# Kernel optimization log

Hardware: AMD Instinct MI355X
Metric: run time of the kernel (lower is better)

The kernel has to match this reference:

```python
import jax, jax.numpy as jnp
import numpy as np

B, G, C, H = 32, 512, 384, 768
TAU = 0.1
ITERS = 10


def _xavier(key, shape):
    fan_in, fan_out = shape
    lim = (6.0 / (fan_in + fan_out)) ** 0.5
    return jax.random.uniform(key, shape, minval=-lim, maxval=lim, dtype=jnp.float32)


def setup_inputs() -> dict:
    key = jax.random.key(0)
    ks = jax.random.split(key, 4)
    return {
        "center_coords": jax.random.normal(ks[0], (B, G, 3), dtype=jnp.float32),
        "group_features": jax.random.normal(ks[1], (B, G, C), dtype=jnp.float32),
        "W1": _xavier(ks[2], (C, H)),
        "b1": jnp.zeros((H,), jnp.float32),
        "W2": _xavier(ks[3], (H, G)),
        "b2": jnp.zeros((G,), jnp.float32),
    }


def _sinkhorn(scores):
    # scores: (B, G, G); log-space Sinkhorn row/col normalization
    log_alpha = scores / TAU
    for _ in range(ITERS):
        log_alpha = log_alpha - jax.nn.logsumexp(log_alpha, axis=-1, keepdims=True)
        log_alpha = log_alpha - jax.nn.logsumexp(log_alpha, axis=-2, keepdims=True)
    return jnp.exp(log_alpha)


def _greedy_assign(P):
    # Equivalent to torch loop: process entries in descending value order,
    # assign (row, col) if both free == repeatedly take global argmax over
    # entries with free row and free col. P: (G, G) -> perm: (G,) int32.
    g = P.shape[-1]
    flat = P.reshape(-1)

    def step(_, carry):
        row_free, col_free, assign = carry
        mask = (row_free[:, None] & col_free[None, :]).reshape(-1)
        idx = jnp.argmax(jnp.where(mask, flat, -jnp.inf))
        r = idx // g
        c = idx % g
        return (row_free.at[r].set(False), col_free.at[c].set(False), assign.at[r].set(c.astype(jnp.int32)))

    init = (jnp.ones((g,), bool), jnp.ones((g,), bool), jnp.full((g,), -1, jnp.int32))
    _, _, assign = jax.lax.fori_loop(0, g, step, init)
    return assign


def _apply_perm(data, perm):
    # reordered[new_pos] = data[orig_pos]; perm[orig_pos] = new_pos
    return jnp.zeros_like(data).at[perm].set(data)


def reference(center_coords, group_features, W1, b1, W2, b2):
    h = jax.nn.relu(jnp.einsum('bgc,ch->bgh', group_features, W1) + b1)
    scores = jnp.einsum('bgh,hk->bgk', h, W2) + b2  # (B, G, G)
    P = _sinkhorn(scores)
    perm_indices = jax.vmap(_greedy_assign)(P)  # (B, G)
    reordered_coords = jax.vmap(_apply_perm)(center_coords, perm_indices)
    reordered_feats = jax.vmap(_apply_perm)(group_features, perm_indices)
    return reordered_coords, reordered_feats, perm_indices
```

## Files before the change

### kernel.cpp

```cpp
#include <hip/hip_runtime.h>
#include <math.h>

#define NB 32
#define NG 512
#define NC 384
#define NH 768

typedef float f32x4v __attribute__((ext_vector_type(4)));
typedef __bf16 bf16_t;
typedef bf16_t bf16x8 __attribute__((ext_vector_type(8)));
typedef bf16_t bf16x4 __attribute__((ext_vector_type(4)));

__device__ __forceinline__ void split3(float x, bf16_t& h, bf16_t& m, bf16_t& lo)
{
    h = (bf16_t)x;
    float r1 = x - (float)h;
    m = (bf16_t)r1;
    float r2 = r1 - (float)m;
    lo = (bf16_t)r2;
}

__global__ __launch_bounds__(256) void presplit_W(
    const float* __restrict__ W, bf16_t* __restrict__ planeB, int K, int N)
{
    int tid = blockIdx.x * 256 + threadIdx.x;
    int nkc = K >> 5;
    if (tid >= nkc * N) return;
    int kc = tid / N;
    int col = tid - kc * N;
    bf16x8 rh[4], rm[4], rl[4];
#pragma unroll
    for (int k = 0; k < 32; k++) {
        float x = W[(size_t)(kc * 32 + k) * N + col];
        bf16_t h, m, lo;
        split3(x, h, m, lo);
        const int s = (k >> 2) & 3;
        const int sub = ((k >> 4) << 2) + (k & 3);
        rh[s][sub] = h; rm[s][sub] = m; rl[s][sub] = lo;
    }
    int swz = (col >> 1) & 3;
    size_t b0 = ((size_t)(kc * 3 + 0) * N + col) * 32;
    size_t b1 = ((size_t)(kc * 3 + 1) * N + col) * 32;
    size_t b2 = ((size_t)(kc * 3 + 2) * N + col) * 32;
#pragma unroll
    for (int s = 0; s < 4; s++) {
        int d = (s ^ swz) << 3;
        *(bf16x8*)&planeB[b0 + d] = rh[s];
        *(bf16x8*)&planeB[b1 + d] = rm[s];
        *(bf16x8*)&planeB[b2 + d] = rl[s];
    }
}

__global__ __launch_bounds__(256, 4) void gemm_bias_mfma(
    const float* __restrict__ A, const bf16_t* __restrict__ planeB,
    const float* __restrict__ bias, float* __restrict__ Co,
    int M, int N, int K, int mode)
{
    __shared__ __align__(16) bf16_t sA[3][64][32];
    int ntiles = N >> 7;
    int cpx = gridDim.x >> 3;
    int bid = blockIdx.x;
    int wg = (bid & 7) * cpx + (bid >> 3);
    int bm = (wg / ntiles) << 6;
    int bn = (wg % ntiles) << 7;
    int t = threadIdx.x;
    int l = t & 63, w = t >> 6;
    int wr = (w >> 1) << 5;
    int wc = (w & 1) << 6;
    int fr = l & 15;
    int fq = l >> 4;

    int sa_row = t >> 2;
    int sa_k0 = (t & 3) << 3;
    int qA = (sa_k0 >> 2) & 3;
    int hsel = (sa_k0 & 16) ? 4 : 0;
    int aswz = (sa_row >> 1) & 3;
    int colQ0 = ((qA ^ aswz) << 3) + hsel;
    int colQ1 = (((qA + 1) ^ aswz) << 3) + hsel;
    const float* apBase = A + (size_t)(bm + sa_row) * K + sa_k0;

    size_t planeStride = (size_t)N << 5;
    int rb0 = wc + 0 * 16 + fr, rb1 = wc + 1 * 16 + fr;
    int rb2 = wc + 2 * 16 + fr, rb3 = wc + 3 * 16 + fr;
    size_t o0 = ((size_t)(bn + rb0) << 5) + ((fq ^ ((rb0 >> 1) & 3)) << 3);
    size_t o1 = ((size_t)(bn + rb1) << 5) + ((fq ^ ((rb1 >> 1) & 3)) << 3);
    size_t o2 = ((size_t)(bn + rb2) << 5) + ((fq ^ ((rb2 >> 1) & 3)) << 3);
    size_t o3 = ((size_t)(bn + rb3) << 5) + ((fq ^ ((rb3 >> 1) & 3)) << 3);

    f32x4v acc[2][4];
#pragma unroll
    for (int i = 0; i < 2; i++)
#pragma unroll
        for (int j = 0; j < 4; j++) acc[i][j] = (f32x4v)(0.f);

    float4 qa0 = *(const float4*)(apBase);
    float4 qa1 = *(const float4*)(apBase + 4);
    bf16x8 b0H = *(const bf16x8*)&planeB[o0];
    bf16x8 b0M = *(const bf16x8*)&planeB[planeStride + o0];
    bf16x8 b0L = *(const bf16x8*)&planeB[2 * planeStride + o0];
    bf16x8 b1H = *(const bf16x8*)&planeB[o1];
    bf16x8 b1M = *(const bf16x8*)&planeB[planeStride + o1];
    bf16x8 b1L = *(const bf16x8*)&planeB[2 * planeStride + o1];

    int nkc = K >> 5;
    for (int kc = 0; kc < K; kc += 32) {
        int kci = kc >> 5;
        int kciN = (kci + 1 < nkc) ? kci + 1 : kci;
        const bf16_t* pb  = planeB + (size_t)(kci * 3) * planeStride;
        const bf16_t* pbn = planeB + (size_t)(kciN * 3) * planeStride;
        __syncthreads();
        {
            float xs[8] = { qa0.x, qa0.y, qa0.z, qa0.w,
                            qa1.x, qa1.y, qa1.z, qa1.w };
            bf16_t hs[8], ms[8], ls[8];
#pragma unroll
            for (int e = 0; e < 8; e++) split3(xs[e], hs[e], ms[e], ls[e]);
            *(bf16x4*)&sA[0][sa_row][colQ0] = (bf16x4){ hs[0], hs[1], hs[2], hs[3] };
            *(bf16x4*)&sA[0][sa_row][colQ1] = (bf16x4){ hs[4], hs[5], hs[6], hs[7] };
            *(bf16x4*)&sA[1][sa_row][colQ0] = (bf16x4){ ms[0], ms[1], ms[2], ms[3] };
            *(bf16x4*)&sA[1][sa_row][colQ1] = (bf16x4){ ms[4], ms[5], ms[6], ms[7] };
            *(bf16x4*)&sA[2][sa_row][colQ0] = (bf16x4){ ls[0], ls[1], ls[2], ls[3] };
            *(bf16x4*)&sA[2][sa_row][colQ1] = (bf16x4){ ls[4], ls[5], ls[6], ls[7] };
        }
        __syncthreads();
        if (kc + 32 < K) {
            const float* ap = apBase + kc + 32;
            qa0 = *(const float4*)(ap);
            qa1 = *(const float4*)(ap + 4);
        }
        bf16x8 b2H = *(const bf16x8*)&pb[o2];
        bf16x8 b2M = *(const bf16x8*)&pb[planeStride + o2];
        bf16x8 b2L = *(const bf16x8*)&pb[2 * planeStride + o2];
        bf16x8 b3H = *(const bf16x8*)&pb[o3];
        bf16x8 b3M = *(const bf16x8*)&pb[planeStride + o3];
        bf16x8 b3L = *(const bf16x8*)&pb[2 * planeStride + o3];
        bf16x8 afH[2], afM[2], afL[2];
#pragma unroll
        for (int i = 0; i < 2; i++) {
            int ra = wr + i * 16 + fr;
            int pk = (fq ^ ((ra >> 1) & 3)) << 3;
            afH[i] = *(const bf16x8*)&sA[0][ra][pk];
            afM[i] = *(const bf16x8*)&sA[1][ra][pk];
            afL[i] = *(const bf16x8*)&sA[2][ra][pk];
        }
#define MFMA6(i, j, BH, BM, BL)                                               \
        acc[i][j] = __builtin_amdgcn_mfma_f32_16x16x32_bf16(                  \
            afH[i], BH, acc[i][j], 0, 0, 0);                                  \
        acc[i][j] = __builtin_amdgcn_mfma_f32_16x16x32_bf16(                  \
            afH[i], BM, acc[i][j], 0, 0, 0);                                  \
        acc[i][j] = __builtin_amdgcn_mfma_f32_16x16x32_bf16(                  \
            afM[i], BH, acc[i][j], 0, 0, 0);                                  \
        acc[i][j] = __builtin_amdgcn_mfma_f32_16x16x32_bf16(                  \
            afM[i], BM, acc[i][j], 0, 0, 0);                                  \
        acc[i][j] = __builtin_amdgcn_mfma_f32_16x16x32_bf16(                  \
            afH[i], BL, acc[i][j], 0, 0, 0);                                  \
        acc[i][j] = __builtin_amdgcn_mfma_f32_16x16x32_bf16(                  \
            afL[i], BH, acc[i][j], 0, 0, 0);
        MFMA6(0, 0, b0H, b0M, b0L)
        MFMA6(1, 0, b0H, b0M, b0L)
        MFMA6(0, 1, b1H, b1M, b1L)
        MFMA6(1, 1, b1H, b1M, b1L)
        b0H = *(const bf16x8*)&pbn[o0];
        b0M = *(const bf16x8*)&pbn[planeStride + o0];
        b0L = *(const bf16x8*)&pbn[2 * planeStride + o0];
        b1H = *(const bf16x8*)&pbn[o1];
        b1M = *(const bf16x8*)&pbn[planeStride + o1];
        b1L = *(const bf16x8*)&pbn[2 * planeStride + o1];
        MFMA6(0, 2, b2H, b2M, b2L)
        MFMA6(1, 2, b2H, b2M, b2L)
        MFMA6(0, 3, b3H, b3M, b3L)
        MFMA6(1, 3, b3H, b3M, b3L)
#undef MFMA6
    }

    int orow = fq << 2;
#pragma unroll
    for (int j = 0; j < 4; j++) {
        int colg = bn + wc + j * 16 + fr;
        float bj = bias[colg];
#pragma unroll
        for (int i = 0; i < 2; i++) {
            int rowg = bm + wr + i * 16 + orow;
#pragma unroll
            for (int r = 0; r < 4; r++) {
                float val = acc[i][j][r] + bj;
                val = (mode == 0) ? fmaxf(val, 0.f) : val / 0.1f;
                Co[(size_t)(rowg + r) * N + colg] = val;
            }
        }
    }
}

#define DPP6_MAXF(x)                                                              \
    { int _t;                                                                     \
      _t = __builtin_amdgcn_update_dpp(__float_as_int(x), __float_as_int(x),      \
               0x111, 0xf, 0xf, false); x = fmaxf(x, __int_as_float(_t));         \
      _t = __builtin_amdgcn_update_dpp(__float_as_int(x), __float_as_int(x),      \
               0x112, 0xf, 0xf, false); x = fmaxf(x, __int_as_float(_t));         \
      _t = __builtin_amdgcn_update_dpp(__float_as_int(x), __float_as_int(x),      \
               0x114, 0xf, 0xf, false); x = fmaxf(x, __int_as_float(_t));         \
      _t = __builtin_amdgcn_update_dpp(__float_as_int(x), __float_as_int(x),      \
               0x118, 0xf, 0xf, false); x = fmaxf(x, __int_as_float(_t));         \
      _t = __builtin_amdgcn_update_dpp(__float_as_int(x), __float_as_int(x),      \
               0x142, 0xa, 0xf, false); x = fmaxf(x, __int_as_float(_t));         \
      _t = __builtin_amdgcn_update_dpp(__float_as_int(x), __float_as_int(x),      \
               0x143, 0xc, 0xf, false); x = fmaxf(x, __int_as_float(_t)); }

#define DPP6_ADDF(x)                                                              \
    { int _t;                                                                     \
      _t = __builtin_amdgcn_update_dpp(__float_as_int(x), __float_as_int(x),      \
               0x111, 0xf, 0xf, false); x = x + __int_as_float(_t);               \
      _t = __builtin_amdgcn_update_dpp(__float_as_int(x), __float_as_int(x),      \
               0x112, 0xf, 0xf, false); x = x + __int_as_float(_t);               \
      _t = __builtin_amdgcn_update_dpp(__float_as_int(x), __float_as_int(x),      \
               0x114, 0xf, 0xf, false); x = x + __int_as_float(_t);               \
      _t = __builtin_amdgcn_update_dpp(__float_as_int(x), __float_as_int(x),      \
               0x118, 0xf, 0xf, false); x = x + __int_as_float(_t);               \
      _t = __builtin_amdgcn_update_dpp(__float_as_int(x), __float_as_int(x),      \
               0x142, 0xa, 0xf, false); x = x + __int_as_float(_t);               \
      _t = __builtin_amdgcn_update_dpp(__float_as_int(x), __float_as_int(x),      \
               0x143, 0xc, 0xf, false); x = x + __int_as_float(_t); }

__global__ __launch_bounds__(512) void sinkhorn_iter_fused(
    const float* __restrict__ A0, float* __restrict__ uu,
    const float* __restrict__ vIn, float* __restrict__ vOut,
    const float* __restrict__ psIn, float* __restrict__ psOut, int first)
{
    int blk = blockIdx.x;
    int b = blk >> 3, rc = blk & 7;
    int t = threadIdx.x;
    int l = t & 63, w = t >> 6;
    __shared__ __align__(16) float svv[512];

    if (first) {
        svv[t] = 0.f;
    } else {
        float S = 0.f;
#pragma unroll
        for (int r8 = 0; r8 < 8; r8++) S += psIn[((b << 3) + r8) * NG + t];
        float nv = vIn[(b << 9) + t] - __logf(S);
        svv[t] = nv;
        if (rc == 0) vOut[(b << 9) + t] = nv;
    }
    __syncthreads();

    float4 v0 = *(const float4*)(&svv[4 * l]);
    float4 v1 = *(const float4*)(&svv[256 + 4 * l]);
    int row0 = (rc << 6) + (w << 3);
    const float* base = A0 + ((size_t)((b << 9) + row0) << 9);

    float cs0 = 0.f, cs1 = 0.f, cs2 = 0.f, cs3 = 0.f;
    float cs4 = 0.f, cs5 = 0.f, cs6 = 0.f, cs7 = 0.f;

    float4 a0 = *(const float4*)(base + 4 * l);
    float4 a1 = *(const float4*)(base + 256 + 4 * l);
    float4 b0 = *(const float4*)(base + (1 << 9) + 4 * l);
    float4 b1 = *(const float4*)(base + (1 << 9) + 256 + 4 * l);

#pragma unroll
    for (int rr = 0; rr < 8; ++rr) {
        float4 c0, c1;
        if (rr < 6) {
            const float* nrow = base + ((size_t)(rr + 2) << 9);
            c0 = *(const float4*)(nrow + 4 * l);
            c1 = *(const float4*)(nrow + 256 + 4 * l);
        }
        float x0 = a0.x + v0.x, x1 = a0.y + v0.y;
        float x2 = a0.z + v0.z, x3 = a0.w + v0.w;
        float x4 = a1.x + v1.x, x5 = a1.y + v1.y;
        float x6 = a1.z + v1.z, x7 = a1.w + v1.w;
        float m = fmaxf(fmaxf(fmaxf(x0, x1), fmaxf(x2, x3)),
                        fmaxf(fmaxf(x4, x5), fmaxf(x6, x7)));
        DPP6_MAXF(m)
        int mi = __builtin_amdgcn_readlane(__float_as_int(m), 63);
        m = __int_as_float(mi);
        float e0 = __expf(x0 - m), e1 = __expf(x1 - m);
        float e2 = __expf(x2 - m), e3 = __expf(x3 - m);
        float e4 = __expf(x4 - m), e5 = __expf(x5 - m);
        float e6 = __expf(x6 - m), e7 = __expf(x7 - m);
        float s = ((e0 + e1) + (e2 + e3)) + ((e4 + e5) + (e6 + e7));
        DPP6_ADDF(s)
        int si = __builtin_amdgcn_readlane(__float_as_int(s), 63);
        s = __int_as_float(si);
        float inv = 1.0f / s;
        cs0 += e0 * inv; cs1 += e1 * inv; cs2 += e2 * inv; cs3 += e3 * inv;
        cs4 += e4 * inv; cs5 += e5 * inv; cs6 += e6 * inv; cs7 += e7 * inv;
        if (l == 63) uu[(b << 9) + row0 + rr] = -(m + __logf(s));
        a0 = b0; a1 = b1;
        b0 = c0; b1 = c1;
    }

    __shared__ float sacc[8][512];
    float4 w0; w0.x = cs0; w0.y = cs1; w0.z = cs2; w0.w = cs3;
    float4 w1; w1.x = cs4; w1.y = cs5; w1.z = cs6; w1.w = cs7;
    *(float4*)&sacc[w][4 * l] = w0;
    *(float4*)&sacc[w][256 + 4 * l] = w1;
    __syncthreads();
    float pA = sacc[0][t] + sacc[1][t] + sacc[2][t] + sacc[3][t]
             + sacc[4][t] + sacc[5][t] + sacc[6][t] + sacc[7][t];
    int o = ((b << 3) + rc) * NG;
    psOut[o + t] = pA;
}

__global__ __launch_bounds__(256) void col_combine_final(
    const float* __restrict__ psIn, const float* __restrict__ vIn,
    float* __restrict__ vOut)
{
    int tid = blockIdx.x * 256 + threadIdx.x;
    int b = tid >> 9, j = tid & 511;
    float S = 0.f;
#pragma unroll
    for (int r8 = 0; r8 < 8; r8++) S += psIn[((b << 3) + r8) * NG + j];
    vOut[tid] = vIn[tid] - __logf(S);
}

__device__ __forceinline__ void masked_row_argmax(
    const float* __restrict__ rowp, int l, unsigned int free8, int rr,
    float& outV, int& outF)
{
    float4 x0 = *(const float4*)(rowp + 8 * l);
    float4 x1 = *(const float4*)(rowp + 8 * l + 4);
    float q0 = (free8 & 1u)   ? x0.x : -1.0f;
    float q1 = (free8 & 2u)   ? x0.y : -1.0f;
    float q2 = (free8 & 4u)   ? x0.z : -1.0f;
    float q3 = (free8 & 8u)   ? x0.w : -1.0f;
    float q4 = (free8 & 16u)  ? x1.x : -1.0f;
    float q5 = (free8 & 32u)  ? x1.y : -1.0f;
    float q6 = (free8 & 64u)  ? x1.z : -1.0f;
    float q7 = (free8 & 128u) ? x1.w : -1.0f;
    float lm = fmaxf(fmaxf(fmaxf(q0, q1), fmaxf(q2, q3)),
                     fmaxf(fmaxf(q4, q5), fmaxf(q6, q7)));
    int sb = (rr << 9) + 8 * l;
    int lf = 0x7FFFFFFF;
    lf = (q7 == lm) ? sb + 7 : lf;
    lf = (q6 == lm) ? sb + 6 : lf;
    lf = (q5 == lm) ? sb + 5 : lf;
    lf = (q4 == lm) ? sb + 4 : lf;
    lf = (q3 == lm) ? sb + 3 : lf;
    lf = (q2 == lm) ? sb + 2 : lf;
    lf = (q1 == lm) ? sb + 1 : lf;
    lf = (q0 == lm) ? sb + 0 : lf;
    float gg = lm;
    DPP6_MAXF(gg)
    int ggi = __builtin_amdgcn_readlane(__float_as_int(gg), 63);
    float g1 = __int_as_float(ggi);
    unsigned long long tb = __ballot(lm == g1);
    int tl = __ffsll(tb) - 1;
    outV = g1;
    outF = __builtin_amdgcn_readlane(lf, tl);
}

__global__ __launch_bounds__(256) void p_rowmax(
    const float* __restrict__ A0, const float* __restrict__ uu,
    const float* __restrict__ vv, float* __restrict__ P,
    int* __restrict__ rbCr, int* __restrict__ rbCc,
    unsigned long long* __restrict__ freeRow,
    unsigned long long* __restrict__ freeCol,
    int* __restrict__ remaining)
{
    if (blockIdx.x == 0) {
        int t = threadIdx.x;
        freeRow[t] = ~0ULL;
        freeCol[t] = ~0ULL;
        if (t < NB) remaining[t] = NG;
    }
    int wrow = blockIdx.x * 4 + (threadIdx.x >> 6);
    int l = threadIdx.x & 63;
    int b = wrow >> 9;
    float ur = uu[wrow];
    const float* vb = vv + (b << 9);
    size_t ro = (size_t)wrow << 9;
    float4 a0 = *(const float4*)(A0 + ro + 8 * l);
    float4 a1 = *(const float4*)(A0 + ro + 8 * l + 4);
    float4 v0 = *(const float4*)(vb + 8 * l);
    float4 v1 = *(const float4*)(vb + 8 * l + 4);
    float p0 = expf(a0.x + ur + v0.x);
    float p1 = expf(a0.y + ur + v0.y);
    float p2 = expf(a0.z + ur + v0.z);
    float p3 = expf(a0.w + ur + v0.w);
    float p4 = expf(a1.x + ur + v1.x);
    float p5 = expf(a1.y + ur + v1.y);
    float p6 = expf(a1.z + ur + v1.z);
    float p7 = expf(a1.w + ur + v1.w);
    float4 o0; o0.x = p0; o0.y = p1; o0.z = p2; o0.w = p3;
    float4 o1; o1.x = p4; o1.y = p5; o1.z = p6; o1.w = p7;
    *(float4*)(P + ro + 8 * l) = o0;
    *(float4*)(P + ro + 8 * l + 4) = o1;
    float mv = fmaxf(fmaxf(fmaxf(p0, p1), fmaxf(p2, p3)),
                     fmaxf(fmaxf(p4, p5), fmaxf(p6, p7)));
    int cb = 8 * l;
    int f = 0x7FFFFFFF;
    f = (p7 == mv) ? cb + 7 : f;
    f = (p6 == mv) ? cb + 6 : f;
    f = (p5 == mv) ? cb + 5 : f;
    f = (p4 == mv) ? cb + 4 : f;
    f = (p3 == mv) ? cb + 3 : f;
    f = (p2 == mv) ? cb + 2 : f;
    f = (p1 == mv) ? cb + 1 : f;
    f = (p0 == mv) ? cb + 0 : f;
    float g = mv;
    DPP6_MAXF(g)
    int gi = __builtin_amdgcn_readlane(__float_as_int(g), 63);
    float gm = __int_as_float(gi);
    unsigned long long tb = __ballot(mv == gm);
    int tl = __ffsll(tb) - 1;
    int bestc = __builtin_amdgcn_readlane(f, tl);
    if (l == 0) { rbCr[wrow] = bestc; rbCc[wrow] = -1; }
}

__global__ __launch_bounds__(512) void mutual_round(
    const float* __restrict__ P, int* __restrict__ rbCr, int* __restrict__ rbCc,
    unsigned long long* __restrict__ freeRow,
    unsigned long long* __restrict__ freeCol,
    int* __restrict__ remaining, int* __restrict__ permInt)
{
    int b = blockIdx.x;
    if (remaining[b] == 0) return;
    int t = threadIdx.x;
    int l = t & 63;
    int w = t >> 6;
    const float* Pb = P + (size_t)b * NG * NG;

    __shared__ unsigned int fr[16], fc[16];
    __shared__ int sRC[NG];
    __shared__ int sCC[NG];
    __shared__ int freeList[NG];
    __shared__ int dirtyRows[NG];
    __shared__ int nFree, nDirtyRow, takeCnt;
    __shared__ int wCnt[8], wOff[8];

    if (t < 8) {
        unsigned long long x = freeRow[b * 8 + t];
        fr[2 * t] = (unsigned)x; fr[2 * t + 1] = (unsigned)(x >> 32);
    } else if (t < 16) {
        int i = t - 8;
        unsigned long long x = freeCol[b * 8 + i];
        fc[2 * i] = (unsigned)x; fc[2 * i + 1] = (unsigned)(x >> 32);
    }
    sRC[t] = rbCr[(b << 9) + t];
    sCC[t] = rbCc[(b << 9) + t];
    if (t == 0) { nDirtyRow = 0; takeCnt = 0; }
    __syncthreads();

    bool isFree = (fr[t >> 5] >> (t & 31)) & 1u;
    unsigned long long bm = __ballot(isFree);
    if (l == 0) wCnt[w] = __popcll(bm);
    if (isFree) {
        int c = sRC[t];
        if (!((fc[c >> 5] >> (c & 31)) & 1u)) {
            int d = atomicAdd(&nDirtyRow, 1);
            dirtyRows[d] = t;
        }
    }
    __syncthreads();
    if (t == 0) {
        int s = 0;
#pragma unroll
        for (int i = 0; i < 8; i++) { wOff[i] = s; s += wCnt[i]; }
        nFree = s;
    }
    __syncthreads();
    if (isFree) {
        int rank = __popcll(bm & ((1ULL << l) - 1ULL));
        freeList[wOff[w] + rank] = t;
    }
    __syncthreads();

    int nd = nDirtyRow;
    for (int d = w; d < nd; d += 8) {
        int r = dirtyRows[d];
        unsigned int free8 = (fc[l >> 2] >> ((l & 3) * 8)) & 0xFFu;
        float nv; int nf;
        masked_row_argmax(Pb + ((size_t)r << 9), l, free8, r, nv, nf);
        if (l == 0) {
            int c = nf & 511;
            sRC[r] = c;
            rbCr[(b << 9) + r] = c;
        }
    }
    __syncthreads();

    bool colFree = (fc[t >> 5] >> (t & 31)) & 1u;
    int cachedR = sCC[t];
    bool colDirty = colFree &&
        (cachedR < 0 || !((fr[cachedR >> 5] >> (cachedR & 31)) & 1u));
    if (colDirty) {
        float best = -1.f; int bestr = 0x7FFFFFFF;
        int nf2 = nFree;
        int i = 0;
        for (; i + 4 <= nf2; i += 4) {
            int r0 = freeList[i], r1 = freeList[i + 1];
            int r2 = freeList[i + 2], r3 = freeList[i + 3];
            float v0 = Pb[((size_t)r0 << 9) + t];
            float v1 = Pb[((size_t)r1 << 9) + t];
            float v2 = Pb[((size_t)r2 << 9) + t];
            float v3 = Pb[((size_t)r3 << 9) + t];
            if (v0 > best) { best = v0; bestr = r0; }
            if (v1 > best) { best = v1; bestr = r1; }
            if (v2 > best) { best = v2; bestr = r2; }
            if (v3 > best) { best = v3; bestr = r3; }
        }
        for (; i < nf2; ++i) {
            int ri = freeList[i];
            float vv2 = Pb[((size_t)ri << 9) + t];
            if (vv2 > best) { best = vv2; bestr = ri; }
        }
        sCC[t] = bestr;
        rbCc[(b << 9) + t] = bestr;
    }
    __syncthreads();

    if (colFree) {
        int r = sCC[t];
        if (r >= 0 && r < NG && sRC[r] == t) {
            permInt[(b << 9) + r] = t;
            atomicAnd(&fr[r >> 5], ~(1u << (r & 31)));
            atomicAnd(&fc[t >> 5], ~(1u << (t & 31)));
            atomicAdd(&takeCnt, 1);
        }
    }
    __syncthreads();
    if (t < 8) {
        freeRow[b * 8 + t] =
            ((unsigned long long)fr[2 * t + 1] << 32) | fr[2 * t];
    } else if (t < 16) {
        int i = t - 8;
        freeCol[b * 8 + i] =
            ((unsigned long long)fc[2 * i + 1] << 32) | fc[2 * i];
    }
    if (t == 0) remaining[b] = remaining[b] - takeCnt;
}

__global__ __launch_bounds__(64) void greedy_cleanup(
    const float* __restrict__ P,
    const unsigned long long* __restrict__ freeRow,
    const unsigned long long* __restrict__ freeCol,
    const int* __restrict__ remaining, int* __restrict__ permInt)
{
    int b = blockIdx.x;
    if (remaining[b] == 0) return;
    int l = threadIdx.x;
    const float* Pb = P + (size_t)b * NG * NG;

    unsigned long long wR = freeRow[b * 8 + (l >> 3)];
    unsigned int myRows = (unsigned int)((wR >> ((l & 7) * 8)) & 0xFF);
    unsigned long long wC = freeCol[b * 8 + (l >> 3)];
    unsigned int free8 = (unsigned int)((wC >> ((l & 7) * 8)) & 0xFF);

    float rv[8]; int rf[8];
#pragma unroll
    for (int k = 0; k < 8; k++) { rv[k] = -1.f; rf[k] = 0x7FFFFFFF; }

    int dmk = (int)myRows;
    unsigned long long act = __ballot(dmk != 0);
    while (act) {
        int src = __ffsll(act) - 1;
        int kk = __ffs(__builtin_amdgcn_readlane(dmk, src)) - 1;
        if (l == src) dmk &= ~(1 << kk);
        int rr = (src << 3) + kk;
        float nv; int nf;
        masked_row_argmax(Pb + ((size_t)rr << 9), l, free8, rr, nv, nf);
        bool upd = (l == src);
        rv[0] = (upd && kk == 0) ? nv : rv[0]; rf[0] = (upd && kk == 0) ? nf : rf[0];
        rv[1] = (upd && kk == 1) ? nv : rv[1]; rf[1] = (upd && kk == 1) ? nf : rf[1];
        rv[2] = (upd && kk == 2) ? nv : rv[2]; rf[2] = (upd && kk == 2) ? nf : rf[2];
        rv[3] = (upd && kk == 3) ? nv : rv[3]; rf[3] = (upd && kk == 3) ? nf : rf[3];
        rv[4] = (upd && kk == 4) ? nv : rv[4]; rf[4] = (upd && kk == 4) ? nf : rf[4];
        rv[5] = (upd && kk == 5) ? nv : rv[5]; rf[5] = (upd && kk == 5) ? nf : rf[5];
        rv[6] = (upd && kk == 6) ? nv : rv[6]; rf[6] = (upd && kk == 6) ? nf : rf[6];
        rv[7] = (upd && kk == 7) ? nv : rv[7]; rf[7] = (upd && kk == 7) ? nf : rf[7];
        act = __ballot(dmk != 0);
    }

    for (int step = 0; step < NG; ++step) {
        float mv = fmaxf(fmaxf(fmaxf(rv[0], rv[1]), fmaxf(rv[2], rv[3])),
                         fmaxf(fmaxf(rv[4], rv[5]), fmaxf(rv[6], rv[7])));
        int f = 0x7FFFFFFF;
        f = (rv[7] == mv) ? rf[7] : f;
        f = (rv[6] == mv) ? rf[6] : f;
        f = (rv[5] == mv) ? rf[5] : f;
        f = (rv[4] == mv) ? rf[4] : f;
        f = (rv[3] == mv) ? rf[3] : f;
        f = (rv[2] == mv) ? rf[2] : f;
        f = (rv[1] == mv) ? rf[1] : f;
        f = (rv[0] == mv) ? rf[0] : f;
        float g = mv;
        DPP6_MAXF(g)
        int gi = __builtin_amdgcn_readlane(__float_as_int(g), 63);
        float gm = __int_as_float(gi);
        if (gm < 0.f) break;
        unsigned long long tb = __ballot(mv == gm);
        int tl = __ffsll(tb) - 1;
        int bestf = __builtin_amdgcn_readlane(f, tl);
        int r = bestf >> 9, c = bestf & 511;
        if (l == 0) permInt[(b << 9) + r] = c;
        if (l == (c >> 3)) free8 &= ~(1u << (c & 7));
        int rl = r - (l << 3);
        int dm2 = 0;
#pragma unroll
        for (int k = 0; k < 8; k++) {
            bool alive = rv[k] >= 0.f;
            bool cm = ((rf[k] ^ c) & 511) == 0;
            bool taken = (rl == k);
            if (taken) rv[k] = -1.f;
            dm2 |= (alive && cm && !taken) ? (1 << k) : 0;
        }
        unsigned long long act2 = __ballot(dm2 != 0);
        while (act2) {
            int src = __ffsll(act2) - 1;
            int kk = __ffs(__builtin_amdgcn_readlane(dm2, src)) - 1;
            if (l == src) dm2 &= ~(1 << kk);
            int rr = (src << 3) + kk;
            float nv; int nf;
            masked_row_argmax(Pb + ((size_t)rr << 9), l, free8, rr, nv, nf);
            bool upd = (l == src);
            rv[0] = (upd && kk == 0) ? nv : rv[0]; rf[0] = (upd && kk == 0) ? nf : rf[0];
            rv[1] = (upd && kk == 1) ? nv : rv[1]; rf[1] = (upd && kk == 1) ? nf : rf[1];
            rv[2] = (upd && kk == 2) ? nv : rv[2]; rf[2] = (upd && kk == 2) ? nf : rf[2];
            rv[3] = (upd && kk == 3) ? nv : rv[3]; rf[3] = (upd && kk == 3) ? nf : rf[3];
            rv[4] = (upd && kk == 4) ? nv : rv[4]; rf[4] = (upd && kk == 4) ? nf : rf[4];
            rv[5] = (upd && kk == 5) ? nv : rv[5]; rf[5] = (upd && kk == 5) ? nf : rf[5];
            rv[6] = (upd && kk == 6) ? nv : rv[6]; rf[6] = (upd && kk == 6) ? nf : rf[6];
            rv[7] = (upd && kk == 7) ? nv : rv[7]; rf[7] = (upd && kk == 7) ? nf : rf[7];
            act2 = __ballot(dm2 != 0);
        }
    }
}

__global__ void scatter_all(const float* __restrict__ coords,
    const float* __restrict__ feats, const int* __restrict__ perm,
    float* __restrict__ dstCoords, float* __restrict__ dstFeats,
    float* __restrict__ permF)
{
    int tid = blockIdx.x * 256 + threadIdx.x;
    int rc = tid / 96;
    int q = tid - rc * 96;
    int b = rc >> 9;
    int p = perm[rc];
    const float4* s4 = (const float4*)(feats + (size_t)rc * NC);
    float4* d4 = (float4*)(dstFeats + ((size_t)(b << 9) + p) * NC);
    d4[q] = s4[q];
    if (q == 0) {
        permF[rc] = (float)p;
        size_t so = (size_t)rc * 3;
        size_t dd = ((size_t)(b << 9) + p) * 3;
        dstCoords[dd] = coords[so];
        dstCoords[dd + 1] = coords[so + 1];
        dstCoords[dd + 2] = coords[so + 2];
    }
}

extern "C" void kernel_launch(void* const* d_in, const int* in_sizes, int n_in,
                              void* d_out, int out_size, void* d_ws, size_t ws_size,
                              hipStream_t stream)
{
    const float* coords = (const float*)d_in[0];
    const float* feats  = (const float*)d_in[1];
    const float* W1 = (const float*)d_in[2];
    const float* b1 = (const float*)d_in[3];
    const float* W2 = (const float*)d_in[4];
    const float* b2 = (const float*)d_in[5];

    float* out = (float*)d_out;
    float* outCoords = out;
    float* outFeats  = out + (size_t)NB * NG * 3;
    float* outPerm   = out + (size_t)NB * NG * 3 + (size_t)NB * NG * NC;

    float* ws = (float*)d_ws;
    float* h   = ws;
    float* A0  = h + (size_t)NB * NG * NH;
    float* u   = A0 + (size_t)NB * NG * NG;
    float* vA  = u + NB * NG;
    float* ps0 = vA + NB * NG;
    float* ps1 = ps0 + NB * 8 * NG;
    int* rbCr  = (int*)(ps1 + NB * 8 * NG);
    int* rbCc  = rbCr + NB * NG;
    unsigned long long* freeRow = (unsigned long long*)(rbCc + NB * NG);
    unsigned long long* freeCol = freeRow + NB * 8;
    int* remaining = (int*)(freeCol + NB * 8);
    int* permInt   = remaining + 32;
    float* vB  = (float*)(permInt + NB * NG);
    bf16_t* pB1 = (bf16_t*)(vB + NB * NG);
    bf16_t* pB2 = pB1 + 12 * 3 * NH * 32;

    const int M = NB * NG;

    presplit_W<<<dim3((12 * NH + 255) / 256), 256, 0, stream>>>(W1, pB1, NC, NH);
    presplit_W<<<dim3((24 * NG + 255) / 256), 256, 0, stream>>>(W2, pB2, NH, NG);

    gemm_bias_mfma<<<dim3((M / 64) * (NH / 128)), 256, 0, stream>>>(
        feats, pB1, b1, h, M, NH, NC, 0);
    gemm_bias_mfma<<<dim3((M / 64) * (NG / 128)), 256, 0, stream>>>(
        h, pB2, b2, A0, M, NG, NH, 1);

    hipMemsetAsync(vA, 0, (size_t)NB * NG * sizeof(float), stream);

    float* pbuf[2] = { ps0, ps1 };
    for (int i = 1; i <= 10; ++i) {
        const float* vin = (i % 2 == 0) ? vA : vB;
        float* vout      = (i % 2 == 0) ? vB : vA;
        const float* pin = pbuf[i & 1];
        float* pout      = pbuf[(i - 1) & 1];
        sinkhorn_iter_fused<<<dim3(NB * 8), 512, 0, stream>>>(
            A0, u, vin, vout, pin, pout, (i == 1) ? 1 : 0);
    }
    col_combine_final<<<dim3(M / 256), 256, 0, stream>>>(pbuf[1], vB, vA);

    float* P = h;
    p_rowmax<<<dim3(M / 4), 256, 0, stream>>>(A0, u, vA, P, rbCr, rbCc,
                                              freeRow, freeCol, remaining);

    for (int r = 0; r < 6; ++r)
        mutual_round<<<dim3(NB), 512, 0, stream>>>(P, rbCr, rbCc, freeRow,
                                                   freeCol, remaining, permInt);

    greedy_cleanup<<<dim3(NB), 64, 0, stream>>>(P, freeRow, freeCol,
                                                remaining, permInt);

    scatter_all<<<dim3((NB * NG * 96) / 256), 256, 0, stream>>>(
        coords, feats, permInt, outCoords, outFeats, outPerm);
}
```

Measured before the change: 342.5 us.

## Emit hidden activations as pre-split bf16 planes and load them directly in GEMM2

The first GEMM's epilogue now splits the ReLU output into three bf16 planes (hi/mid/lo) in a K-chunked layout instead of writing fp32. A new second GEMM reads those planes straight from global memory into registers, without LDS staging or on-the-fly splitting. The aim is to drop the split arithmetic and LDS traffic from the larger second GEMM. In exchange, the first GEMM's epilogue does scattered 2-byte stores, and the second GEMM loses shared-memory reuse of A across waves and has no software prefetch.

```diff
diff --git a/kernel.cpp b/kernel.cpp
--- a/kernel.cpp
+++ b/kernel.cpp
@@ -51,10 +51,10 @@
     }
 }
 
-__global__ __launch_bounds__(256, 4) void gemm_bias_mfma(
+__global__ __launch_bounds__(256, 4) void gemm1_planes(
     const float* __restrict__ A, const bf16_t* __restrict__ planeB,
-    const float* __restrict__ bias, float* __restrict__ Co,
-    int M, int N, int K, int mode)
+    const float* __restrict__ bias, bf16_t* __restrict__ planeOut,
+    int M, int N, int K)
 {
     __shared__ __align__(16) bf16_t sA[3][64][32];
     int ntiles = N >> 7;
@@ -174,17 +174,124 @@
     }
 
     int orow = fq << 2;
+    size_t aM32 = (size_t)M << 5;
 #pragma unroll
     for (int j = 0; j < 4; j++) {
         int colg = bn + wc + j * 16 + fr;
         float bj = bias[colg];
+        int kc2 = ((bn + wc) >> 5) + (j >> 1);
+        int off = (((fr >> 2) & 3) << 3) + ((j & 1) << 2) + (fr & 3);
+        size_t pbase = (size_t)(kc2 * 3) * aM32 + off;
 #pragma unroll
         for (int i = 0; i < 2; i++) {
             int rowg = bm + wr + i * 16 + orow;
 #pragma unroll
             for (int r = 0; r < 4; r++) {
-                float val = acc[i][j][r] + bj;
-                val = (mode == 0) ? fmaxf(val, 0.f) : val / 0.1f;
+                float val = fmaxf(acc[i][j][r] + bj, 0.f);
+                bf16_t hh, mm, ll;
+                split3(val, hh, mm, ll);
+                size_t ad = pbase + ((size_t)(rowg + r) << 5);
+                planeOut[ad] = hh;
+                planeOut[ad + aM32] = mm;
+                planeOut[ad + 2 * aM32] = ll;
+            }
+        }
+    }
+}
+
+__global__ __launch_bounds__(256, 4) void gemm2_direct(
+    const bf16_t* __restrict__ planeA, const bf16_t* __restrict__ planeB,
+    const float* __restrict__ bias, float* __restrict__ Co,
+    int M, int N, int K)
+{
+    int ntiles = N >> 7;
+    int cpx = gridDim.x >> 3;
+    int bid = blockIdx.x;
+    int wg = (bid & 7) * cpx + (bid >> 3);
+    int bm = (wg / ntiles) << 6;
+    int bn = (wg % ntiles) << 7;
+    int t = threadIdx.x;
+    int l = t & 63, w = t >> 6;
+    int wr = (w >> 1) << 5;
+    int wc = (w & 1) << 6;
+    int fr = l & 15;
+    int fq = l >> 4;
+
+    size_t planeStride = (size_t)N << 5;
+    size_t aStride = (size_t)M << 5;
+    size_t aOff0 = ((size_t)(bm + wr + fr) << 5) + (fq << 3);
+    size_t aOff1 = ((size_t)(bm + wr + 16 + fr) << 5) + (fq << 3);
+
+    int rb0 = wc + 0 * 16 + fr, rb1 = wc + 1 * 16 + fr;
+    int rb2 = wc + 2 * 16 + fr, rb3 = wc + 3 * 16 + fr;
+    size_t o0 = ((size_t)(bn + rb0) << 5) + ((fq ^ ((rb0 >> 1) & 3)) << 3);
+    size_t o1 = ((size_t)(bn + rb1) << 5) + ((fq ^ ((rb1 >> 1) & 3)) << 3);
+    size_t o2 = ((size_t)(bn + rb2) << 5) + ((fq ^ ((rb2 >> 1) & 3)) << 3);
+    size_t o3 = ((size_t)(bn + rb3) << 5) + ((fq ^ ((rb3 >> 1) & 3)) << 3);
+
+    f32x4v acc[2][4];
+#pragma unroll
+    for (int i = 0; i < 2; i++)
+#pragma unroll
+        for (int j = 0; j < 4; j++) acc[i][j] = (f32x4v)(0.f);
+
+    int nkc = K >> 5;
+    for (int kci = 0; kci < nkc; ++kci) {
+        const bf16_t* pa = planeA + (size_t)(kci * 3) * aStride;
+        const bf16_t* pb = planeB + (size_t)(kci * 3) * planeStride;
+        bf16x8 aH0 = *(const bf16x8*)&pa[aOff0];
+        bf16x8 aM0 = *(const bf16x8*)&pa[aStride + aOff0];
+        bf16x8 aL0 = *(const bf16x8*)&pa[2 * aStride + aOff0];
+        bf16x8 aH1 = *(const bf16x8*)&pa[aOff1];
+        bf16x8 aM1 = *(const bf16x8*)&pa[aStride + aOff1];
+        bf16x8 aL1 = *(const bf16x8*)&pa[2 * aStride + aOff1];
+        bf16x8 b0H = *(const bf16x8*)&pb[o0];
+        bf16x8 b0M = *(const bf16x8*)&pb[planeStride + o0];
+        bf16x8 b0L = *(const bf16x8*)&pb[2 * planeStride + o0];
+        bf16x8 b1H = *(const bf16x8*)&pb[o1];
+        bf16x8 b1M = *(const bf16x8*)&pb[planeStride + o1];
+        bf16x8 b1L = *(const bf16x8*)&pb[2 * planeStride + o1];
+        bf16x8 b2H = *(const bf16x8*)&pb[o2];
+        bf16x8 b2M = *(const bf16x8*)&pb[planeStride + o2];
+        bf16x8 b2L = *(const bf16x8*)&pb[2 * planeStride + o2];
+        bf16x8 b3H = *(const bf16x8*)&pb[o3];
+        bf16x8 b3M = *(const bf16x8*)&pb[planeStride + o3];
+        bf16x8 b3L = *(const bf16x8*)&pb[2 * planeStride + o3];
+#define MFMA6D(i, j, AH, AM, AL, BH, BM, BL)                                  \
+        acc[i][j] = __builtin_amdgcn_mfma_f32_16x16x32_bf16(                  \
+            AH, BH, acc[i][j], 0, 0, 0);                                      \
+        acc[i][j] = __builtin_amdgcn_mfma_f32_16x16x32_bf16(                  \
+            AH, BM, acc[i][j], 0, 0, 0);                                      \
+        acc[i][j] = __builtin_amdgcn_mfma_f32_16x16x32_bf16(                  \
+            AM, BH, acc[i][j], 0, 0, 0);                                      \
+        acc[i][j] = __builtin_amdgcn_mfma_f32_16x16x32_bf16(                  \
+            AM, BM, acc[i][j], 0, 0, 0);                                      \
+        acc[i][j] = __builtin_amdgcn_mfma_f32_16x16x32_bf16(                  \
+            AH, BL, acc[i][j], 0, 0, 0);                                      \
+        acc[i][j] = __builtin_amdgcn_mfma_f32_16x16x32_bf16(                  \
+            AL, BH, acc[i][j], 0, 0, 0);
+        MFMA6D(0, 0, aH0, aM0, aL0, b0H, b0M, b0L)
+        MFMA6D(1, 0, aH1, aM1, aL1, b0H, b0M, b0L)
+        MFMA6D(0, 1, aH0, aM0, aL0, b1H, b1M, b1L)
+        MFMA6D(1, 1, aH1, aM1, aL1, b1H, b1M, b1L)
+        MFMA6D(0, 2, aH0, aM0, aL0, b2H, b2M, b2L)
+        MFMA6D(1, 2, aH1, aM1, aL1, b2H, b2M, b2L)
+        MFMA6D(0, 3, aH0, aM0, aL0, b3H, b3M, b3L)
+        MFMA6D(1, 3, aH1, aM1, aL1, b3H, b3M, b3L)
+#undef MFMA6D
+    }
+
+    int orow = fq << 2;
+#pragma unroll
+    for (int j = 0; j < 4; j++) {
+        int colg = bn + wc + j * 16 + fr;
+        float bj = bias[colg];
+#pragma unroll
+        for (int i = 0; i < 2; i++) {
+            int rowg = bm + wr + i * 16 + orow;
+#pragma unroll
+            for (int r = 0; r < 4; r++) {
+                float val = (acc[i][j][r] + bj) / 0.1f;
                 Co[(size_t)(rowg + r) * N + colg] = val;
             }
         }
@@ -666,34 +773,33 @@
     float* outFeats  = out + (size_t)NB * NG * 3;
     float* outPerm   = out + (size_t)NB * NG * 3 + (size_t)NB * NG * NC;
 
-    float* ws = (float*)d_ws;
-    float* h   = ws;
-    float* A0  = h + (size_t)NB * NG * NH;
-    float* u   = A0 + (size_t)NB * NG * NG;
-    float* vA  = u + NB * NG;
-    float* ps0 = vA + NB * NG;
+    const int M = NB * NG;
+
+    bf16_t* pA2 = (bf16_t*)d_ws;
+    float* A0  = (float*)(pA2 + (size_t)(NH / 32) * 3 * M * 32);
+    float* u   = A0 + (size_t)M * NG;
+    float* vA  = u + M;
+    float* ps0 = vA + M;
     float* ps1 = ps0 + NB * 8 * NG;
     int* rbCr  = (int*)(ps1 + NB * 8 * NG);
-    int* rbCc  = rbCr + NB * NG;
-    unsigned long long* freeRow = (unsigned long long*)(rbCc + NB * NG);
+    int* rbCc  = rbCr + M;
+    unsigned long long* freeRow = (unsigned long long*)(rbCc + M);
     unsigned long long* freeCol = freeRow + NB * 8;
     int* remaining = (int*)(freeCol + NB * 8);
     int* permInt   = remaining + 32;
-    float* vB  = (float*)(permInt + NB * NG);
-    bf16_t* pB1 = (bf16_t*)(vB + NB * NG);
+    float* vB  = (float*)(permInt + M);
+    bf16_t* pB1 = (bf16_t*)(vB + M);
     bf16_t* pB2 = pB1 + 12 * 3 * NH * 32;
-
-    const int M = NB * NG;
 
     presplit_W<<<dim3((12 * NH + 255) / 256), 256, 0, stream>>>(W1, pB1, NC, NH);
     presplit_W<<<dim3((24 * NG + 255) / 256), 256, 0, stream>>>(W2, pB2, NH, NG);
 
-    gemm_bias_mfma<<<dim3((M / 64) * (NH / 128)), 256, 0, stream>>>(
-        feats, pB1, b1, h, M, NH, NC, 0);
-    gemm_bias_mfma<<<dim3((M / 64) * (NG / 128)), 256, 0, stream>>>(
-        h, pB2, b2, A0, M, NG, NH, 1);
-
-    hipMemsetAsync(vA, 0, (size_t)NB * NG * sizeof(float), stream);
+    gemm1_planes<<<dim3((M / 64) * (NH / 128)), 256, 0, stream>>>(
+        feats, pB1, b1, pA2, M, NH, NC);
+    gemm2_direct<<<dim3((M / 64) * (NG / 128)), 256, 0, stream>>>(
+        pA2, pB2, b2, A0, M, NG, NH);
+
+    hipMemsetAsync(vA, 0, (size_t)M * sizeof(float), stream);
 
     float* pbuf[2] = { ps0, ps1 };
     for (int i = 1; i <= 10; ++i) {
@@ -706,7 +812,7 @@
     }
     col_combine_final<<<dim3(M / 256), 256, 0, stream>>>(pbuf[1], vB, vA);
 
-    float* P = h;
+    float* P = (float*)pA2;
     p_rowmax<<<dim3(M / 4), 256, 0, stream>>>(A0, u, vA, P, rbCr, rbCc,
                                               freeRow, freeCol, remaining);
 
```

After: 350.6 us. +2.4%, slower.
